# Kernel tuning notes

Measured on AMD Instinct MI355X. Metric: run time of the kernel, lower is better.

Reference implementation:

```python
import jax, jax.numpy as jnp
import numpy as np

SHAPES = ((100, 100), (50, 50), (25, 25))  # (H, W) per level
B, D, NH, HD, NL, NP, DFF = 4, 256, 8, 32, 3, 4, 1024
L = sum(h * w for h, w in SHAPES)  # 13125
EPS = 1e-5


def _layer_norm(x, g, b):
    m = jnp.mean(x, axis=-1, keepdims=True)
    v = jnp.var(x, axis=-1, keepdims=True)
    return (x - m) * jax.lax.rsqrt(v + EPS) * g + b


def _grid_sample_bilinear(img, grid):
    """img: [N,C,H,W]; grid: [N,Lq,P,2] in [-1,1]; align_corners=False, zero pad.
    Returns [N,C,Lq,P]."""
    N, C, H, W = img.shape
    x = ((grid[..., 0] + 1.0) * W - 1.0) * 0.5
    y = ((grid[..., 1] + 1.0) * H - 1.0) * 0.5
    x0 = jnp.floor(x); y0 = jnp.floor(y)
    x1 = x0 + 1.0; y1 = y0 + 1.0
    wx1 = x - x0; wx0 = 1.0 - wx1
    wy1 = y - y0; wy0 = 1.0 - wy1
    flat = img.reshape(N, C, H * W)

    def gather(ix, iy):
        valid = ((ix >= 0) & (ix < W) & (iy >= 0) & (iy < H)).astype(img.dtype)
        ii = (jnp.clip(iy, 0, H - 1).astype(jnp.int32) * W
              + jnp.clip(ix, 0, W - 1).astype(jnp.int32))  # [N,Lq,P]
        idx = jnp.broadcast_to(ii.reshape(N, 1, -1), (N, C, ii.shape[1] * ii.shape[2]))
        vals = jnp.take_along_axis(flat, idx, axis=2).reshape(N, C, ii.shape[1], ii.shape[2])
        return vals * valid[:, None]

    out = (gather(x0, y0) * (wx0 * wy0)[:, None]
           + gather(x1, y0) * (wx1 * wy0)[:, None]
           + gather(x0, y1) * (wx0 * wy1)[:, None]
           + gather(x1, y1) * (wx1 * wy1)[:, None])
    return out


def _ms_deform_attn_core(value, loc, attn):
    """value: [B,L,NH,HD]; loc: [B,Lq,NH,NL,NP,2] in [0,1]; attn: [B,Lq,NH,NL,NP]."""
    Bn, Lq = loc.shape[0], loc.shape[1]
    grids = 2.0 * loc - 1.0
    start = 0
    samples = []
    for lid, (H, W) in enumerate(SHAPES):
        v = value[:, start:start + H * W]            # [B,HW,NH,HD]
        start += H * W
        v = v.transpose(0, 2, 3, 1).reshape(Bn * NH, HD, H, W)
        g = grids[:, :, :, lid].transpose(0, 2, 1, 3, 4).reshape(Bn * NH, Lq, NP, 2)
        samples.append(_grid_sample_bilinear(v, g))  # [B*NH,HD,Lq,NP]
    sv = jnp.stack(samples, axis=-2).reshape(Bn * NH, HD, Lq, NL * NP)
    a = attn.transpose(0, 2, 1, 3, 4).reshape(Bn * NH, 1, Lq, NL * NP)
    out = (sv * a).sum(-1)                            # [B*NH,HD,Lq]
    return out.reshape(Bn, NH * HD, Lq).transpose(0, 2, 1)


def setup_inputs() -> dict:
    key = jax.random.key(0)
    ks = jax.random.split(key, 16)
    f32 = jnp.float32
    inp = {
        'src': jax.random.normal(ks[0], (B, L, D), f32),
        'pos': jax.random.normal(ks[1], (B, L, D), f32),
        'reference_points': jax.random.uniform(ks[2], (B, L, NL, 2), f32),
        'Wv': jax.random.normal(ks[3], (D, D), f32) * 0.02,
        'bv': jnp.zeros((D,), f32),
        'Woff': jax.random.normal(ks[4], (D, NH * NL * NP * 2), f32) * 0.02,
        'boff': jax.random.normal(ks[5], (NH * NL * NP * 2,), f32) * 0.5,
        'Wattn': jax.random.normal(ks[6], (D, NH * NL * NP), f32) * 0.02,
        'battn': jnp.zeros((NH * NL * NP,), f32),
        'Wout': jax.random.normal(ks[7], (D, D), f32) * 0.02,
        'bout': jnp.zeros((D,), f32),
        'g1': jnp.ones((D,), f32), 'b1': jnp.zeros((D,), f32),
        'Wff1': jax.random.normal(ks[8], (D, DFF), f32) * 0.02,
        'bff1': jnp.zeros((DFF,), f32),
        'Wff2': jax.random.normal(ks[9], (DFF, D), f32) * 0.02,
        'bff2': jnp.zeros((D,), f32),
        'g2': jnp.ones((D,), f32), 'b2': jnp.zeros((D,), f32),
    }
    return inp


def reference(src, pos, reference_points, Wv, bv, Woff, boff, Wattn, battn,
              Wout, bout, g1, b1, Wff1, bff1, Wff2, bff2, g2, b2):
    # DeformableTransformerEncoderLayer forward (eval mode: dropout = identity)
    q = src + pos
    value = (src @ Wv + bv).reshape(B, L, NH, HD)
    off = (q @ Woff + boff).reshape(B, L, NH, NL, NP, 2)
    attn = jax.nn.softmax((q @ Wattn + battn).reshape(B, L, NH, NL * NP), axis=-1)
    attn = attn.reshape(B, L, NH, NL, NP)
    norm = jnp.array([[w, h] for h, w in SHAPES], dtype=src.dtype)  # [NL,2] = (W,H)
    loc = reference_points[:, :, None, :, None, :] + off / norm[None, None, None, :, None, :]
    attn_out = _ms_deform_attn_core(value, loc, attn) @ Wout + bout
    x = _layer_norm(src + attn_out, g1, b1)
    ff = jax.nn.relu(x @ Wff1 + bff1) @ Wff2 + bff2
    return _layer_norm(x + ff, g2, b2)
```

## Files before the change

### kernel.cpp

```cpp
#include <hip/hip_runtime.h>


#define BLTOK 52500
#define MP    52608
#define LSP   13125

using short8  = __attribute__((ext_vector_type(8))) short;
using ushort8v= __attribute__((ext_vector_type(8))) unsigned short;
using f32x4   = __attribute__((ext_vector_type(4))) float;
using fl2     = __attribute__((ext_vector_type(2))) float;

__device__ __forceinline__ ushort f2b(float f) {
  union { float f; unsigned u; } x; x.f = f;
  unsigned r = (x.u + 0x7fffu + ((x.u >> 16) & 1u)) >> 16;
  return (ushort)r;
}
__device__ __forceinline__ float b2f(ushort h) {
  union { unsigned u; float f; } x; x.u = ((unsigned)h) << 16;
  return x.f;
}

#define GLDS16(gp, lp) __builtin_amdgcn_global_load_lds( \
    (const __attribute__((address_space(1))) void*)(gp), \
    (__attribute__((address_space(3))) void*)(lp), 16, 0, 0)

__global__ __launch_bounds__(256) void prep_weights(
    const float* __restrict__ Wv, const float* __restrict__ Woff,
    const float* __restrict__ Wattn, const float* __restrict__ Wout,
    const float* __restrict__ Wff1, const float* __restrict__ Wff2,
    const float* __restrict__ boff, const float* __restrict__ battn,
    ushort* __restrict__ wv_t, ushort* __restrict__ wcat_t,
    ushort* __restrict__ wout_t, ushort* __restrict__ wff1_t,
    ushort* __restrict__ wff2_t, float* __restrict__ bcat)
{
  int i = blockIdx.x * 256 + threadIdx.x;
  if (i < 65536) {
    int n = i >> 8, k = i & 255;
    wv_t[i] = f2b(Wv[k * 256 + n]);
    return;
  }
  int j = i - 65536;
  if (j < 98304) {
    int n = j >> 8, k = j & 255;
    float v = (n < 192) ? Woff[k * 192 + n]
            : (n < 288) ? Wattn[k * 96 + (n - 192)] : 0.f;
    wcat_t[j] = f2b(v);
    return;
  }
  j -= 98304;
  if (j < 65536) {
    int n = j >> 8, k = j & 255;
    wout_t[j] = f2b(Wout[k * 256 + n]);
    return;
  }
  j -= 65536;
  if (j < 262144) {
    int n = j >> 8, k = j & 255;
    wff1_t[j] = f2b(Wff1[k * 1024 + n]);
    return;
  }
  j -= 262144;
  if (j < 262144) {
    int n = j >> 10, k = j & 1023;
    wff2_t[j] = f2b(Wff2[k * 256 + n]);
    return;
  }
  j -= 262144;
  if (j < 384) bcat[j] = (j < 192) ? boff[j] : (j < 288) ? battn[j - 192] : 0.f;
}

__global__ __launch_bounds__(256) void prep_act(
    const float* __restrict__ src, const float* __restrict__ pos,
    ushort* __restrict__ src_bf, ushort* __restrict__ q_bf)
{
  const size_t e = ((size_t)blockIdx.x * 256 + threadIdx.x) * 4;
  if (e >= (size_t)MP * 256) return;
  ushort4 sb, qb;
  if (e < (size_t)BLTOK * 256) {
    const float4 s = *(const float4*)(src + e);
    const float4 p = *(const float4*)(pos + e);
    sb.x = f2b(s.x); sb.y = f2b(s.y); sb.z = f2b(s.z); sb.w = f2b(s.w);
    qb.x = f2b(s.x + p.x); qb.y = f2b(s.y + p.y);
    qb.z = f2b(s.z + p.z); qb.w = f2b(s.w + p.w);
  } else {
    sb.x = sb.y = sb.z = sb.w = 0;
    qb.x = qb.y = qb.z = qb.w = 0;
  }
  *(ushort4*)(src_bf + e) = sb;
  *(ushort4*)(q_bf + e) = qb;
}

template <int EPI>
__global__ __launch_bounds__(256) void gemm128(
    const ushort* __restrict__ A, const ushort* __restrict__ Bt,
    const float* __restrict__ bias, const float* __restrict__ addf,
    const ushort* __restrict__ addb, ushort* __restrict__ C,
    int Mact, int Nact, int Nstr, int K)
{
  __shared__ __align__(16) ushort sm[16384];
  ushort* As = sm;
  ushort* Bs = sm + 8192;
  float*  epf = (float*)sm;
  const int tid = threadIdx.x;
  const int wave = tid >> 6, lane = tid & 63;
  const int n0 = blockIdx.x * 128, m0 = blockIdx.y * 128;
  const int srow = lane >> 2, skc = (lane & 3) * 8;
  const ushort* Ag = A + (size_t)(m0 + wave * 32 + srow) * K + skc;
  const ushort* Bg = Bt + (size_t)(n0 + wave * 32 + srow) * K + skc;
  const int quad = lane >> 4, l16 = lane & 15;
  const int wm = (wave & 1) * 64, wn = (wave >> 1) * 64;
  f32x4 acc[4][4] = {};

#define STAGE(buf, kk) { \
    ushort* la = As + (buf) * 4096 + wave * 1024; \
    ushort* lb = Bs + (buf) * 4096 + wave * 1024; \
    GLDS16(Ag + (kk), la); \
    GLDS16(Ag + (kk) + 16 * K, la + 512); \
    GLDS16(Bg + (kk), lb); \
    GLDS16(Bg + (kk) + 16 * K, lb + 512); }

  STAGE(0, 0);
  int cur = 0;
  for (int k0 = 0; k0 < K; k0 += 32) {
    __syncthreads();
    if (k0 + 32 < K) STAGE(cur ^ 1, k0 + 32);
    const ushort* Ab = As + cur * 4096;
    const ushort* Bb = Bs + cur * 4096;
    short8 af[4], bf[4];
#pragma unroll
    for (int i = 0; i < 4; i++)
      af[i] = *(const short8*)(&Ab[(wm + i * 16 + l16) * 32 + quad * 8]);
#pragma unroll
    for (int j = 0; j < 4; j++)
      bf[j] = *(const short8*)(&Bb[(wn + j * 16 + l16) * 32 + quad * 8]);
#pragma unroll
    for (int i = 0; i < 4; i++)
#pragma unroll
      for (int j = 0; j < 4; j++)
        acc[i][j] = __builtin_amdgcn_mfma_f32_16x16x32_bf16(af[i], bf[j],
                                                            acc[i][j], 0, 0, 0);
    cur ^= 1;
  }
#undef STAGE

  for (int half = 0; half < 2; half++) {
    __syncthreads();
    if ((wave & 1) == half) {
#pragma unroll
      for (int i = 0; i < 4; i++)
#pragma unroll
        for (int j = 0; j < 4; j++)
#pragma unroll
          for (int r = 0; r < 4; r++)
            epf[(i * 16 + quad * 4 + r) * 128 + wn + j * 16 + l16] = acc[i][j][r];
    }
    __syncthreads();
    const int gm0 = m0 + half * 64;
#pragma unroll
    for (int g = 0; g < 4; g++) {
      const int lrow = g * 16 + (tid >> 4);
      const int col0 = (tid & 15) * 8;
      const int grow = gm0 + lrow;
      const int gcol = n0 + col0;
      if (grow < Mact && gcol < Nact) {
        float v[8];
#pragma unroll
        for (int c = 0; c < 8; c++) v[c] = epf[lrow * 128 + col0 + c] + bias[gcol + c];
        const size_t idx = (size_t)grow * Nstr + gcol;
        if (EPI == 1) {
          const float4 a0 = *(const float4*)(addf + idx);
          const float4 a1 = *(const float4*)(addf + idx + 4);
          v[0] += a0.x; v[1] += a0.y; v[2] += a0.z; v[3] += a0.w;
          v[4] += a1.x; v[5] += a1.y; v[6] += a1.z; v[7] += a1.w;
        }
        if (EPI == 2) {
#pragma unroll
          for (int c = 0; c < 8; c++) v[c] = fmaxf(v[c], 0.f);
        }
        if (EPI == 3) {
          const ushort8v ab = *(const ushort8v*)(addb + idx);
#pragma unroll
          for (int c = 0; c < 8; c++) v[c] += b2f(ab[c]);
        }
        ushort8v o;
#pragma unroll
        for (int c = 0; c < 8; c++) o[c] = f2b(v[c]);
        *(ushort8v*)(C + idx) = o;
      }
    }
  }
}

__global__ __launch_bounds__(256) void softmax12(ushort* __restrict__ offattn)
{
  const int t = blockIdx.x * 256 + threadIdx.x;
  if (t >= BLTOK * 8) return;
  const int r = t >> 3, h = t & 7;
  ushort* p = offattn + (size_t)r * 320 + 192 + h * 12;
  float v[12], mx = -1e30f;
#pragma unroll
  for (int i = 0; i < 12; i++) { v[i] = b2f(p[i]); mx = fmaxf(mx, v[i]); }
  float s = 0.f;
#pragma unroll
  for (int i = 0; i < 12; i++) { v[i] = expf(v[i] - mx); s += v[i]; }
  const float inv = 1.f / s;
#pragma unroll
  for (int i = 0; i < 12; i++) p[i] = f2b(v[i] * inv);
}

__global__ __launch_bounds__(256) void deform_sample(
    const ushort* __restrict__ value, const ushort* __restrict__ oa_all,
    const float* __restrict__ refp, ushort* __restrict__ outb)
{
  const int tid = threadIdx.x;
  const int tok = blockIdx.x * 8 + (tid >> 5);
  if (tok >= BLTOK) return;
  const int b = tok / LSP;
  const int l = tid & 31;
  const int h = l >> 2;
  const ushort* oa = oa_all + (uint)tok * 320u;
  const float* rp = refp + (uint)tok * 6u;
  const uint base = (uint)b * (LSP * 256u) + (uint)(l * 8);
  const int Wl[3] = {100, 50, 25};
  const int Stl[3] = {0, 10000, 12500};
  fl2 acc2[4] = {};
#pragma unroll
  for (int lid = 0; lid < 3; lid++) {
    const int W = Wl[lid], st = Stl[lid];
    const float Wf = (float)W;
    const float rx = rp[lid * 2], ry = rp[lid * 2 + 1];
#pragma unroll
    for (int p = 0; p < 4; p++) {
      const uint oxy = *(const uint*)(oa + h * 24 + lid * 8 + p * 2);
      union { uint u; float f; } ux, uy;
      ux.u = oxy << 16;
      uy.u = oxy & 0xffff0000u;
      const float aw = b2f(oa[192 + h * 12 + lid * 4 + p]);
      const float x = (rx + ux.f / Wf) * Wf - 0.5f;
      const float y = (ry + uy.f / Wf) * Wf - 0.5f;
      const float x0f = floorf(x), y0f = floorf(y);
      const float wx1 = x - x0f, wy1 = y - y0f;
      const float wx0 = 1.f - wx1, wy0 = 1.f - wy1;
      const int ix0 = (int)x0f, iy0 = (int)y0f;
      const bool x0v = (ix0 >= 0) & (ix0 < W);
      const bool x1v = (ix0 + 1 >= 0) & (ix0 + 1 < W);
      const bool y0v = (iy0 >= 0) & (iy0 < W);
      const bool y1v = (iy0 + 1 >= 0) & (iy0 + 1 < W);
      const float ay0 = aw * wy0, ay1 = aw * wy1;
      const float w00 = (x0v & y0v) ? ay0 * wx0 : 0.f;
      const float w10 = (x1v & y0v) ? ay0 * wx1 : 0.f;
      const float w01 = (x0v & y1v) ? ay1 * wx0 : 0.f;
      const float w11 = (x1v & y1v) ? ay1 * wx1 : 0.f;
      const int ix0c = min(max(ix0, 0), W - 1);
      const int ix1c = min(max(ix0 + 1, 0), W - 1);
      const int iy0c = min(max(iy0, 0), W - 1);
      const int iy1c = min(max(iy0 + 1, 0), W - 1);
      const uint r00 = (uint)(st + iy0c * W + ix0c) * 256u;
      const uint r10 = (uint)(st + iy0c * W + ix1c) * 256u;
      const uint r01 = (uint)(st + iy1c * W + ix0c) * 256u;
      const uint r11 = (uint)(st + iy1c * W + ix1c) * 256u;
      const uint4 q00 = *(const uint4*)(value + base + r00);
      const uint4 q10 = *(const uint4*)(value + base + r10);
      const uint4 q01 = *(const uint4*)(value + base + r01);
      const uint4 q11 = *(const uint4*)(value + base + r11);
      const fl2 w00v = {w00, w00}, w10v = {w10, w10};
      const fl2 w01v = {w01, w01}, w11v = {w11, w11};
      const uint* u00 = (const uint*)&q00;
      const uint* u10 = (const uint*)&q10;
      const uint* u01 = (const uint*)&q01;
      const uint* u11 = (const uint*)&q11;
#pragma unroll
      for (int pp = 0; pp < 4; pp++) {
        union { uint u; float f; } a, bb2, cc, dd, a2, b2u, c2, d2;
        a.u  = u00[pp] << 16;  a2.u  = u00[pp] & 0xffff0000u;
        bb2.u= u10[pp] << 16;  b2u.u = u10[pp] & 0xffff0000u;
        cc.u = u01[pp] << 16;  c2.u  = u01[pp] & 0xffff0000u;
        dd.u = u11[pp] << 16;  d2.u  = u11[pp] & 0xffff0000u;
        fl2 v00 = {a.f, a2.f}, v10 = {bb2.f, b2u.f};
        fl2 v01 = {cc.f, c2.f}, v11 = {dd.f, d2.f};
        acc2[pp] += w00v * v00 + w10v * v10 + w01v * v01 + w11v * v11;
      }
    }
  }
  ushort4 o0, o1;
  o0.x = f2b(acc2[0].x); o0.y = f2b(acc2[0].y);
  o0.z = f2b(acc2[1].x); o0.w = f2b(acc2[1].y);
  o1.x = f2b(acc2[2].x); o1.y = f2b(acc2[2].y);
  o1.z = f2b(acc2[3].x); o1.w = f2b(acc2[3].y);
  ushort* op = outb + (uint)tok * 256u + (uint)(l * 8);
  *(ushort4*)op = o0;
  *(ushort4*)(op + 4) = o1;
}

template <int OUTF>
__global__ __launch_bounds__(256) void ln256(
    const ushort* __restrict__ in, const float* __restrict__ gg,
    const float* __restrict__ bb, ushort* __restrict__ outb,
    float* __restrict__ outf, int rows)
{
  const int wave = threadIdx.x >> 6, lane = threadIdx.x & 63;
  const int r = blockIdx.x * 4 + wave;
  if (r >= rows) return;
  const ushort* rowp = in + (size_t)r * 256;
  const ushort4 u = *(const ushort4*)(rowp + lane * 4);
  float v[4] = {b2f(u.x), b2f(u.y), b2f(u.z), b2f(u.w)};
  float s = v[0] + v[1] + v[2] + v[3];
  float s2 = v[0] * v[0] + v[1] * v[1] + v[2] * v[2] + v[3] * v[3];
#pragma unroll
  for (int o = 32; o > 0; o >>= 1) {
    s += __shfl_xor(s, o);
    s2 += __shfl_xor(s2, o);
  }
  const float mean = s * (1.f / 256.f);
  const float var = s2 * (1.f / 256.f) - mean * mean;
  const float rstd = rsqrtf(var + 1e-5f);
#pragma unroll
  for (int j = 0; j < 4; j++) {
    const int col = lane * 4 + j;
    const float o = (v[j] - mean) * rstd * gg[col] + bb[col];
    if (OUTF) outf[(size_t)r * 256 + col] = o;
    else outb[(size_t)r * 256 + col] = f2b(o);
  }
}

extern "C" void kernel_launch(void* const* d_in, const int* in_sizes, int n_in,
                              void* d_out, int out_size, void* d_ws, size_t ws_size,
                              hipStream_t stream)
{
  const float* src   = (const float*)d_in[0];
  const float* pos   = (const float*)d_in[1];
  const float* refp  = (const float*)d_in[2];
  const float* Wv    = (const float*)d_in[3];
  const float* bv    = (const float*)d_in[4];
  const float* Woff  = (const float*)d_in[5];
  const float* boff  = (const float*)d_in[6];
  const float* Wattn = (const float*)d_in[7];
  const float* battn = (const float*)d_in[8];
  const float* Wout  = (const float*)d_in[9];
  const float* bout  = (const float*)d_in[10];
  const float* g1    = (const float*)d_in[11];
  const float* b1    = (const float*)d_in[12];
  const float* Wff1  = (const float*)d_in[13];
  const float* bff1  = (const float*)d_in[14];
  const float* Wff2  = (const float*)d_in[15];
  const float* bff2  = (const float*)d_in[16];
  const float* g2    = (const float*)d_in[17];
  const float* b2    = (const float*)d_in[18];
  float* out = (float*)d_out;
  char* ws = (char*)d_ws;

  ushort* wcat_t = (ushort*)(ws + 0);
  ushort* wff1_t = (ushort*)(ws + 196608);
  ushort* wff2_t = (ushort*)(ws + 720896);
  float*  bcat   = (float*)(ws + 1245184);
  ushort* A1 = (ushort*)(ws + 1246720);
  ushort* A2 = (ushort*)(ws + 28182016);
  ushort* A3 = (ushort*)(ws + 55117312);
  ushort* A4 = (ushort*)(ws + 81997312);
  ushort* A5 = (ushort*)(ws + 115597312);
  ushort* wout_t = (ushort*)(ws + 223076352);
  ushort* wv_t   = (ushort*)(ws + 223207424);

  prep_weights<<<2946, 256, 0, stream>>>(Wv, Woff, Wattn, Wout, Wff1, Wff2,
                                         boff, battn,
                                         wv_t, wcat_t, wout_t, wff1_t, wff2_t, bcat);
  prep_act<<<MP / 4, 256, 0, stream>>>(src, pos, A1, A2);
  gemm128<0><<<dim3(2, MP / 128), 256, 0, stream>>>(A1, wv_t, bv, nullptr, nullptr,
                                                    A3, BLTOK, 256, 256, 256);
  gemm128<0><<<dim3(3, MP / 128), 256, 0, stream>>>(A2, wcat_t, bcat, nullptr, nullptr,
                                                    A4, BLTOK, 320, 320, 256);
  softmax12<<<(BLTOK * 8 + 255) / 256, 256, 0, stream>>>(A4);
  deform_sample<<<(BLTOK + 7) / 8, 256, 0, stream>>>(A3, A4, refp, A5);
  gemm128<3><<<dim3(2, MP / 128), 256, 0, stream>>>(A5, wout_t, bout, nullptr, A1,
                                                    A4, BLTOK, 256, 256, 256);
  ln256<0><<<BLTOK / 4, 256, 0, stream>>>(A4, g1, b1, A2, nullptr, BLTOK);
  gemm128<2><<<dim3(8, MP / 128), 256, 0, stream>>>(A2, wff1_t, bff1, nullptr, nullptr,
                                                    A5, MP, 1024, 1024, 256);
  gemm128<3><<<dim3(2, MP / 128), 256, 0, stream>>>(A5, wff2_t, bff2, nullptr, A2,
                                                    A3, BLTOK, 256, 256, 1024);
  ln256<1><<<BLTOK / 4, 256, 0, stream>>>(A3, g2, b2, nullptr, out, BLTOK);
}
```

Measured before the change: 484.3 us.

## Fuse softmax into deform sampling and remap threads to one head each

Removes the separate softmax12 kernel and computes the per-head softmax over the 12 attention logits inside deform_sample. Each thread now handles one head's 32 channels of one token instead of 8 channels, so offsets, weights and bilinear indices are computed once per head rather than four times. The location math is simplified to ref*W - 0.5 + offset. Blocks are reordered so each group stays within one batch, which should help L2 locality. The trade-off is higher register pressure (16 accumulators plus 16-byte loads per corner) and a different memory access pattern for the value gathers.

```diff
diff --git a/kernel.cpp b/kernel.cpp
--- a/kernel.cpp
+++ b/kernel.cpp
@@ -18,6 +18,12 @@
 __device__ __forceinline__ float b2f(ushort h) {
   union { unsigned u; float f; } x; x.u = ((unsigned)h) << 16;
   return x.f;
+}
+__device__ __forceinline__ float lo16f(uint u) {
+  union { unsigned u; float f; } x; x.u = u << 16; return x.f;
+}
+__device__ __forceinline__ float hi16f(uint u) {
+  union { unsigned u; float f; } x; x.u = u & 0xffff0000u; return x.f;
 }
 
 #define GLDS16(gp, lp) __builtin_amdgcn_global_load_lds( \
@@ -191,53 +197,66 @@
   }
 }
 
-__global__ __launch_bounds__(256) void softmax12(ushort* __restrict__ offattn)
-{
-  const int t = blockIdx.x * 256 + threadIdx.x;
-  if (t >= BLTOK * 8) return;
-  const int r = t >> 3, h = t & 7;
-  ushort* p = offattn + (size_t)r * 320 + 192 + h * 12;
-  float v[12], mx = -1e30f;
-#pragma unroll
-  for (int i = 0; i < 12; i++) { v[i] = b2f(p[i]); mx = fmaxf(mx, v[i]); }
-  float s = 0.f;
-#pragma unroll
-  for (int i = 0; i < 12; i++) { v[i] = expf(v[i] - mx); s += v[i]; }
-  const float inv = 1.f / s;
-#pragma unroll
-  for (int i = 0; i < 12; i++) p[i] = f2b(v[i] * inv);
-}
-
 __global__ __launch_bounds__(256) void deform_sample(
     const ushort* __restrict__ value, const ushort* __restrict__ oa_all,
     const float* __restrict__ refp, ushort* __restrict__ outb)
 {
   const int tid = threadIdx.x;
-  const int tok = blockIdx.x * 8 + (tid >> 5);
-  if (tok >= BLTOK) return;
-  const int b = tok / LSP;
-  const int l = tid & 31;
-  const int h = l >> 2;
-  const ushort* oa = oa_all + (uint)tok * 320u;
-  const float* rp = refp + (uint)tok * 6u;
-  const uint base = (uint)b * (LSP * 256u) + (uint)(l * 8);
+  const int g = blockIdx.x & 7, j = blockIdx.x >> 3;
+  const int batch = g >> 1;
+  const int tin = ((g & 1) * 206 + j) * 32 + (tid >> 3);
+  if (tin >= LSP) return;
+  const int tok = batch * LSP + tin;
+  const int h = tid & 7;
+  const ushort* oa = oa_all + (size_t)tok * 320;
+  uint offv[12];
+  {
+    const uint4 o0 = *(const uint4*)(oa + h * 24);
+    const uint4 o1 = *(const uint4*)(oa + h * 24 + 8);
+    const uint4 o2 = *(const uint4*)(oa + h * 24 + 16);
+    offv[0] = o0.x; offv[1] = o0.y; offv[2] = o0.z; offv[3] = o0.w;
+    offv[4] = o1.x; offv[5] = o1.y; offv[6] = o1.z; offv[7] = o1.w;
+    offv[8] = o2.x; offv[9] = o2.y; offv[10] = o2.z; offv[11] = o2.w;
+  }
+  float wsm[12];
+  {
+    const ushort* lg = oa + 192 + h * 12;
+    const uint2 l0 = *(const uint2*)(lg);
+    const uint2 l1 = *(const uint2*)(lg + 4);
+    const uint2 l2 = *(const uint2*)(lg + 8);
+    wsm[0] = lo16f(l0.x); wsm[1] = hi16f(l0.x);
+    wsm[2] = lo16f(l0.y); wsm[3] = hi16f(l0.y);
+    wsm[4] = lo16f(l1.x); wsm[5] = hi16f(l1.x);
+    wsm[6] = lo16f(l1.y); wsm[7] = hi16f(l1.y);
+    wsm[8] = lo16f(l2.x); wsm[9] = hi16f(l2.x);
+    wsm[10] = lo16f(l2.y); wsm[11] = hi16f(l2.y);
+    float mx = wsm[0];
+#pragma unroll
+    for (int i = 1; i < 12; i++) mx = fmaxf(mx, wsm[i]);
+    float s = 0.f;
+#pragma unroll
+    for (int i = 0; i < 12; i++) { wsm[i] = __expf(wsm[i] - mx); s += wsm[i]; }
+    const float inv = 1.f / s;
+#pragma unroll
+    for (int i = 0; i < 12; i++) wsm[i] *= inv;
+  }
+  const float* rp = refp + (size_t)tok * 6;
+  const uint vbase = (uint)batch * (LSP * 256u) + (uint)(h * 32);
   const int Wl[3] = {100, 50, 25};
   const int Stl[3] = {0, 10000, 12500};
-  fl2 acc2[4] = {};
+  fl2 acc2[16] = {};
 #pragma unroll
   for (int lid = 0; lid < 3; lid++) {
     const int W = Wl[lid], st = Stl[lid];
     const float Wf = (float)W;
-    const float rx = rp[lid * 2], ry = rp[lid * 2 + 1];
+    const float bx = rp[lid * 2] * Wf - 0.5f;
+    const float by = rp[lid * 2 + 1] * Wf - 0.5f;
 #pragma unroll
     for (int p = 0; p < 4; p++) {
-      const uint oxy = *(const uint*)(oa + h * 24 + lid * 8 + p * 2);
-      union { uint u; float f; } ux, uy;
-      ux.u = oxy << 16;
-      uy.u = oxy & 0xffff0000u;
-      const float aw = b2f(oa[192 + h * 12 + lid * 4 + p]);
-      const float x = (rx + ux.f / Wf) * Wf - 0.5f;
-      const float y = (ry + uy.f / Wf) * Wf - 0.5f;
+      const uint oxy = offv[lid * 4 + p];
+      const float x = bx + lo16f(oxy);
+      const float y = by + hi16f(oxy);
+      const float aw = wsm[lid * 4 + p];
       const float x0f = floorf(x), y0f = floorf(y);
       const float wx1 = x - x0f, wy1 = y - y0f;
       const float wx0 = 1.f - wx1, wy0 = 1.f - wy1;
@@ -255,41 +274,63 @@
       const int ix1c = min(max(ix0 + 1, 0), W - 1);
       const int iy0c = min(max(iy0, 0), W - 1);
       const int iy1c = min(max(iy0 + 1, 0), W - 1);
-      const uint r00 = (uint)(st + iy0c * W + ix0c) * 256u;
-      const uint r10 = (uint)(st + iy0c * W + ix1c) * 256u;
-      const uint r01 = (uint)(st + iy1c * W + ix0c) * 256u;
-      const uint r11 = (uint)(st + iy1c * W + ix1c) * 256u;
-      const uint4 q00 = *(const uint4*)(value + base + r00);
-      const uint4 q10 = *(const uint4*)(value + base + r10);
-      const uint4 q01 = *(const uint4*)(value + base + r01);
-      const uint4 q11 = *(const uint4*)(value + base + r11);
+      const uint r00 = vbase + (uint)(st + iy0c * W + ix0c) * 256u;
+      const uint r10 = vbase + (uint)(st + iy0c * W + ix1c) * 256u;
+      const uint r01 = vbase + (uint)(st + iy1c * W + ix0c) * 256u;
+      const uint r11 = vbase + (uint)(st + iy1c * W + ix1c) * 256u;
+      uint4 q00[2], q10[2], q01[2], q11[2];
+#pragma unroll
+      for (int c = 0; c < 2; c++) {
+        q00[c] = *(const uint4*)(value + r00 + c * 8);
+        q10[c] = *(const uint4*)(value + r10 + c * 8);
+        q01[c] = *(const uint4*)(value + r01 + c * 8);
+        q11[c] = *(const uint4*)(value + r11 + c * 8);
+      }
       const fl2 w00v = {w00, w00}, w10v = {w10, w10};
       const fl2 w01v = {w01, w01}, w11v = {w11, w11};
-      const uint* u00 = (const uint*)&q00;
-      const uint* u10 = (const uint*)&q10;
-      const uint* u01 = (const uint*)&q01;
-      const uint* u11 = (const uint*)&q11;
-#pragma unroll
-      for (int pp = 0; pp < 4; pp++) {
-        union { uint u; float f; } a, bb2, cc, dd, a2, b2u, c2, d2;
-        a.u  = u00[pp] << 16;  a2.u  = u00[pp] & 0xffff0000u;
-        bb2.u= u10[pp] << 16;  b2u.u = u10[pp] & 0xffff0000u;
-        cc.u = u01[pp] << 16;  c2.u  = u01[pp] & 0xffff0000u;
-        dd.u = u11[pp] << 16;  d2.u  = u11[pp] & 0xffff0000u;
-        fl2 v00 = {a.f, a2.f}, v10 = {bb2.f, b2u.f};
-        fl2 v01 = {cc.f, c2.f}, v11 = {dd.f, d2.f};
-        acc2[pp] += w00v * v00 + w10v * v10 + w01v * v01 + w11v * v11;
+      const uint* u00 = (const uint*)q00;
+      const uint* u10 = (const uint*)q10;
+      const uint* u01 = (const uint*)q01;
+      const uint* u11 = (const uint*)q11;
+#pragma unroll
+      for (int d = 0; d < 8; d++) {
+        fl2 v00 = {lo16f(u00[d]), hi16f(u00[d])};
+        fl2 v10 = {lo16f(u10[d]), hi16f(u10[d])};
+        fl2 v01 = {lo16f(u01[d]), hi16f(u01[d])};
+        fl2 v11 = {lo16f(u11[d]), hi16f(u11[d])};
+        acc2[d] += w00v * v00 + w10v * v10 + w01v * v01 + w11v * v11;
+      }
+      uint4 q00b[2], q10b[2], q01b[2], q11b[2];
+#pragma unroll
+      for (int c = 0; c < 2; c++) {
+        q00b[c] = *(const uint4*)(value + r00 + 16 + c * 8);
+        q10b[c] = *(const uint4*)(value + r10 + 16 + c * 8);
+        q01b[c] = *(const uint4*)(value + r01 + 16 + c * 8);
+        q11b[c] = *(const uint4*)(value + r11 + 16 + c * 8);
+      }
+      const uint* v00p = (const uint*)q00b;
+      const uint* v10p = (const uint*)q10b;
+      const uint* v01p = (const uint*)q01b;
+      const uint* v11p = (const uint*)q11b;
+#pragma unroll
+      for (int d = 0; d < 8; d++) {
+        fl2 v00 = {lo16f(v00p[d]), hi16f(v00p[d])};
+        fl2 v10 = {lo16f(v10p[d]), hi16f(v10p[d])};
+        fl2 v01 = {lo16f(v01p[d]), hi16f(v01p[d])};
+        fl2 v11 = {lo16f(v11p[d]), hi16f(v11p[d])};
+        acc2[8 + d] += w00v * v00 + w10v * v10 + w01v * v01 + w11v * v11;
       }
     }
   }
-  ushort4 o0, o1;
-  o0.x = f2b(acc2[0].x); o0.y = f2b(acc2[0].y);
-  o0.z = f2b(acc2[1].x); o0.w = f2b(acc2[1].y);
-  o1.x = f2b(acc2[2].x); o1.y = f2b(acc2[2].y);
-  o1.z = f2b(acc2[3].x); o1.w = f2b(acc2[3].y);
-  ushort* op = outb + (uint)tok * 256u + (uint)(l * 8);
-  *(ushort4*)op = o0;
-  *(ushort4*)(op + 4) = o1;
+  uint ov[16];
+#pragma unroll
+  for (int d = 0; d < 16; d++)
+    ov[d] = (uint)f2b(acc2[d].x) | ((uint)f2b(acc2[d].y) << 16);
+  ushort* op = outb + (size_t)tok * 256 + h * 32;
+  *(uint4*)(op) = *(uint4*)(ov);
+  *(uint4*)(op + 8) = *(uint4*)(ov + 4);
+  *(uint4*)(op + 16) = *(uint4*)(ov + 8);
+  *(uint4*)(op + 24) = *(uint4*)(ov + 12);
 }
 
 template <int OUTF>
@@ -369,8 +410,7 @@
                                                     A3, BLTOK, 256, 256, 256);
   gemm128<0><<<dim3(3, MP / 128), 256, 0, stream>>>(A2, wcat_t, bcat, nullptr, nullptr,
                                                     A4, BLTOK, 320, 320, 256);
-  softmax12<<<(BLTOK * 8 + 255) / 256, 256, 0, stream>>>(A4);
-  deform_sample<<<(BLTOK + 7) / 8, 256, 0, stream>>>(A3, A4, refp, A5);
+  deform_sample<<<8 * 206, 256, 0, stream>>>(A3, A4, refp, A5);
   gemm128<3><<<dim3(2, MP / 128), 256, 0, stream>>>(A5, wout_t, bout, nullptr, A1,
                                                     A4, BLTOK, 256, 256, 256);
   ln256<0><<<BLTOK / 4, 256, 0, stream>>>(A4, g1, b1, A2, nullptr, BLTOK);
```

After: 607.3 us. 25.4% more time.

## Switch GEMMs to 64x256 tiles, trim M padding, simplify deform sampling math

Applied to the files above, without the earlier changes.

Replaces the 128x128 GEMM tile with a 64x256 tile in which each of the four waves owns a 64x64 slice and all waves share one A tile. M padding shrinks to a multiple of 64, and prep_act no longer writes zero padding rows. Padded rows now hold stale workspace data, and the bias-concat GEMM reads weight rows past its real extent; both are masked only by the output bounds checks. The softmax switches to the fast __expf intrinsic, and the deformable sampler precomputes the reference offset per level so it no longer divides and multiplies by W for each point.

```diff
diff --git a/kernel.cpp b/kernel.cpp
--- a/kernel.cpp
+++ b/kernel.cpp
@@ -2,7 +2,7 @@
 
 
 #define BLTOK 52500
-#define MP    52608
+#define MPAD  52544
 #define LSP   13125
 
 using short8  = __attribute__((ext_vector_type(8))) short;
@@ -18,6 +18,12 @@
 __device__ __forceinline__ float b2f(ushort h) {
   union { unsigned u; float f; } x; x.u = ((unsigned)h) << 16;
   return x.f;
+}
+__device__ __forceinline__ float lo16f(uint u) {
+  union { unsigned u; float f; } x; x.u = u << 16; return x.f;
+}
+__device__ __forceinline__ float hi16f(uint u) {
+  union { unsigned u; float f; } x; x.u = u & 0xffff0000u; return x.f;
 }
 
 #define GLDS16(gp, lp) __builtin_amdgcn_global_load_lds( \
@@ -74,62 +80,56 @@
     ushort* __restrict__ src_bf, ushort* __restrict__ q_bf)
 {
   const size_t e = ((size_t)blockIdx.x * 256 + threadIdx.x) * 4;
-  if (e >= (size_t)MP * 256) return;
+  const float4 s = *(const float4*)(src + e);
+  const float4 p = *(const float4*)(pos + e);
   ushort4 sb, qb;
-  if (e < (size_t)BLTOK * 256) {
-    const float4 s = *(const float4*)(src + e);
-    const float4 p = *(const float4*)(pos + e);
-    sb.x = f2b(s.x); sb.y = f2b(s.y); sb.z = f2b(s.z); sb.w = f2b(s.w);
-    qb.x = f2b(s.x + p.x); qb.y = f2b(s.y + p.y);
-    qb.z = f2b(s.z + p.z); qb.w = f2b(s.w + p.w);
-  } else {
-    sb.x = sb.y = sb.z = sb.w = 0;
-    qb.x = qb.y = qb.z = qb.w = 0;
-  }
+  sb.x = f2b(s.x); sb.y = f2b(s.y); sb.z = f2b(s.z); sb.w = f2b(s.w);
+  qb.x = f2b(s.x + p.x); qb.y = f2b(s.y + p.y);
+  qb.z = f2b(s.z + p.z); qb.w = f2b(s.w + p.w);
   *(ushort4*)(src_bf + e) = sb;
   *(ushort4*)(q_bf + e) = qb;
 }
 
 template <int EPI>
-__global__ __launch_bounds__(256) void gemm128(
+__global__ __launch_bounds__(256) void gemm64n(
     const ushort* __restrict__ A, const ushort* __restrict__ Bt,
-    const float* __restrict__ bias, const float* __restrict__ addf,
-    const ushort* __restrict__ addb, ushort* __restrict__ C,
-    int Mact, int Nact, int Nstr, int K)
-{
-  __shared__ __align__(16) ushort sm[16384];
+    const float* __restrict__ bias, const ushort* __restrict__ addb,
+    ushort* __restrict__ C, int Mact, int Nact, int Nstr, int K)
+{
+  __shared__ __align__(16) ushort sm[20480];
   ushort* As = sm;
-  ushort* Bs = sm + 8192;
+  ushort* Bs = sm + 4096;
   float*  epf = (float*)sm;
   const int tid = threadIdx.x;
   const int wave = tid >> 6, lane = tid & 63;
-  const int n0 = blockIdx.x * 128, m0 = blockIdx.y * 128;
+  const int n0 = blockIdx.x * 256, m0 = blockIdx.y * 64;
   const int srow = lane >> 2, skc = (lane & 3) * 8;
-  const ushort* Ag = A + (size_t)(m0 + wave * 32 + srow) * K + skc;
-  const ushort* Bg = Bt + (size_t)(n0 + wave * 32 + srow) * K + skc;
+  const ushort* Ag = A + (size_t)(m0 + wave * 16 + srow) * K + skc;
+  const ushort* Bg = Bt + (size_t)(n0 + wave * 64 + srow) * K + skc;
   const int quad = lane >> 4, l16 = lane & 15;
-  const int wm = (wave & 1) * 64, wn = (wave >> 1) * 64;
+  const int wn = wave * 64;
   f32x4 acc[4][4] = {};
 
 #define STAGE(buf, kk) { \
-    ushort* la = As + (buf) * 4096 + wave * 1024; \
-    ushort* lb = Bs + (buf) * 4096 + wave * 1024; \
+    ushort* la = As + (buf) * 2048 + wave * 512; \
+    ushort* lb = Bs + (buf) * 8192 + wave * 2048; \
     GLDS16(Ag + (kk), la); \
-    GLDS16(Ag + (kk) + 16 * K, la + 512); \
     GLDS16(Bg + (kk), lb); \
-    GLDS16(Bg + (kk) + 16 * K, lb + 512); }
+    GLDS16(Bg + (kk) + 16 * K, lb + 512); \
+    GLDS16(Bg + (kk) + 32 * K, lb + 1024); \
+    GLDS16(Bg + (kk) + 48 * K, lb + 1536); }
 
   STAGE(0, 0);
   int cur = 0;
   for (int k0 = 0; k0 < K; k0 += 32) {
     __syncthreads();
     if (k0 + 32 < K) STAGE(cur ^ 1, k0 + 32);
-    const ushort* Ab = As + cur * 4096;
-    const ushort* Bb = Bs + cur * 4096;
+    const ushort* Ab = As + cur * 2048;
+    const ushort* Bb = Bs + cur * 8192;
     short8 af[4], bf[4];
 #pragma unroll
     for (int i = 0; i < 4; i++)
-      af[i] = *(const short8*)(&Ab[(wm + i * 16 + l16) * 32 + quad * 8]);
+      af[i] = *(const short8*)(&Ab[(i * 16 + l16) * 32 + quad * 8]);
 #pragma unroll
     for (int j = 0; j < 4; j++)
       bf[j] = *(const short8*)(&Bb[(wn + j * 16 + l16) * 32 + quad * 8]);
@@ -143,36 +143,29 @@
   }
 #undef STAGE
 
-  for (int half = 0; half < 2; half++) {
+  for (int q = 0; q < 2; q++) {
     __syncthreads();
-    if ((wave & 1) == half) {
-#pragma unroll
-      for (int i = 0; i < 4; i++)
-#pragma unroll
-        for (int j = 0; j < 4; j++)
-#pragma unroll
-          for (int r = 0; r < 4; r++)
-            epf[(i * 16 + quad * 4 + r) * 128 + wn + j * 16 + l16] = acc[i][j][r];
+#pragma unroll
+    for (int ii = 0; ii < 2; ii++) {
+      const int i = q * 2 + ii;
+#pragma unroll
+      for (int j = 0; j < 4; j++)
+#pragma unroll
+        for (int r = 0; r < 4; r++)
+          epf[(ii * 16 + quad * 4 + r) * 256 + wn + j * 16 + l16] = acc[i][j][r];
     }
     __syncthreads();
-    const int gm0 = m0 + half * 64;
 #pragma unroll
     for (int g = 0; g < 4; g++) {
-      const int lrow = g * 16 + (tid >> 4);
-      const int col0 = (tid & 15) * 8;
-      const int grow = gm0 + lrow;
+      const int lrow = g * 8 + (tid >> 5);
+      const int col0 = (tid & 31) * 8;
+      const int grow = m0 + q * 32 + lrow;
       const int gcol = n0 + col0;
       if (grow < Mact && gcol < Nact) {
         float v[8];
 #pragma unroll
-        for (int c = 0; c < 8; c++) v[c] = epf[lrow * 128 + col0 + c] + bias[gcol + c];
+        for (int c = 0; c < 8; c++) v[c] = epf[lrow * 256 + col0 + c] + bias[gcol + c];
         const size_t idx = (size_t)grow * Nstr + gcol;
-        if (EPI == 1) {
-          const float4 a0 = *(const float4*)(addf + idx);
-          const float4 a1 = *(const float4*)(addf + idx + 4);
-          v[0] += a0.x; v[1] += a0.y; v[2] += a0.z; v[3] += a0.w;
-          v[4] += a1.x; v[5] += a1.y; v[6] += a1.z; v[7] += a1.w;
-        }
         if (EPI == 2) {
 #pragma unroll
           for (int c = 0; c < 8; c++) v[c] = fmaxf(v[c], 0.f);
@@ -202,7 +195,7 @@
   for (int i = 0; i < 12; i++) { v[i] = b2f(p[i]); mx = fmaxf(mx, v[i]); }
   float s = 0.f;
 #pragma unroll
-  for (int i = 0; i < 12; i++) { v[i] = expf(v[i] - mx); s += v[i]; }
+  for (int i = 0; i < 12; i++) { v[i] = __expf(v[i] - mx); s += v[i]; }
   const float inv = 1.f / s;
 #pragma unroll
   for (int i = 0; i < 12; i++) p[i] = f2b(v[i] * inv);
@@ -228,16 +221,14 @@
   for (int lid = 0; lid < 3; lid++) {
     const int W = Wl[lid], st = Stl[lid];
     const float Wf = (float)W;
-    const float rx = rp[lid * 2], ry = rp[lid * 2 + 1];
+    const float bx = rp[lid * 2] * Wf - 0.5f;
+    const float by = rp[lid * 2 + 1] * Wf - 0.5f;
 #pragma unroll
     for (int p = 0; p < 4; p++) {
       const uint oxy = *(const uint*)(oa + h * 24 + lid * 8 + p * 2);
-      union { uint u; float f; } ux, uy;
-      ux.u = oxy << 16;
-      uy.u = oxy & 0xffff0000u;
       const float aw = b2f(oa[192 + h * 12 + lid * 4 + p]);
-      const float x = (rx + ux.f / Wf) * Wf - 0.5f;
-      const float y = (ry + uy.f / Wf) * Wf - 0.5f;
+      const float x = bx + lo16f(oxy);
+      const float y = by + hi16f(oxy);
       const float x0f = floorf(x), y0f = floorf(y);
       const float wx1 = x - x0f, wy1 = y - y0f;
       const float wx0 = 1.f - wx1, wy0 = 1.f - wy1;
@@ -271,13 +262,10 @@
       const uint* u11 = (const uint*)&q11;
 #pragma unroll
       for (int pp = 0; pp < 4; pp++) {
-        union { uint u; float f; } a, bb2, cc, dd, a2, b2u, c2, d2;
-        a.u  = u00[pp] << 16;  a2.u  = u00[pp] & 0xffff0000u;
-        bb2.u= u10[pp] << 16;  b2u.u = u10[pp] & 0xffff0000u;
-        cc.u = u01[pp] << 16;  c2.u  = u01[pp] & 0xffff0000u;
-        dd.u = u11[pp] << 16;  d2.u  = u11[pp] & 0xffff0000u;
-        fl2 v00 = {a.f, a2.f}, v10 = {bb2.f, b2u.f};
-        fl2 v01 = {cc.f, c2.f}, v11 = {dd.f, d2.f};
+        fl2 v00 = {lo16f(u00[pp]), hi16f(u00[pp])};
+        fl2 v10 = {lo16f(u10[pp]), hi16f(u10[pp])};
+        fl2 v01 = {lo16f(u01[pp]), hi16f(u01[pp])};
+        fl2 v11 = {lo16f(u11[pp]), hi16f(u11[pp])};
         acc2[pp] += w00v * v00 + w10v * v10 + w01v * v01 + w11v * v11;
       }
     }
@@ -354,29 +342,29 @@
   ushort* wff2_t = (ushort*)(ws + 720896);
   float*  bcat   = (float*)(ws + 1245184);
   ushort* A1 = (ushort*)(ws + 1246720);
-  ushort* A2 = (ushort*)(ws + 28182016);
-  ushort* A3 = (ushort*)(ws + 55117312);
-  ushort* A4 = (ushort*)(ws + 81997312);
-  ushort* A5 = (ushort*)(ws + 115597312);
-  ushort* wout_t = (ushort*)(ws + 223076352);
-  ushort* wv_t   = (ushort*)(ws + 223207424);
+  ushort* A2 = (ushort*)(ws + 28126720);
+  ushort* A3 = (ushort*)(ws + 55006720);
+  ushort* A4 = (ushort*)(ws + 81886720);
+  ushort* A5 = (ushort*)(ws + 115486720);
+  ushort* wv_t   = (ushort*)(ws + 155486720);
+  ushort* wout_t = (ushort*)(ws + 155617792);
 
   prep_weights<<<2946, 256, 0, stream>>>(Wv, Woff, Wattn, Wout, Wff1, Wff2,
                                          boff, battn,
                                          wv_t, wcat_t, wout_t, wff1_t, wff2_t, bcat);
-  prep_act<<<MP / 4, 256, 0, stream>>>(src, pos, A1, A2);
-  gemm128<0><<<dim3(2, MP / 128), 256, 0, stream>>>(A1, wv_t, bv, nullptr, nullptr,
-                                                    A3, BLTOK, 256, 256, 256);
-  gemm128<0><<<dim3(3, MP / 128), 256, 0, stream>>>(A2, wcat_t, bcat, nullptr, nullptr,
-                                                    A4, BLTOK, 320, 320, 256);
+  prep_act<<<BLTOK / 4, 256, 0, stream>>>(src, pos, A1, A2);
+  gemm64n<0><<<dim3(1, MPAD / 64), 256, 0, stream>>>(A1, wv_t, bv, nullptr,
+                                                     A3, BLTOK, 256, 256, 256);
+  gemm64n<0><<<dim3(2, MPAD / 64), 256, 0, stream>>>(A2, wcat_t, bcat, nullptr,
+                                                     A4, BLTOK, 320, 320, 256);
   softmax12<<<(BLTOK * 8 + 255) / 256, 256, 0, stream>>>(A4);
   deform_sample<<<(BLTOK + 7) / 8, 256, 0, stream>>>(A3, A4, refp, A5);
-  gemm128<3><<<dim3(2, MP / 128), 256, 0, stream>>>(A5, wout_t, bout, nullptr, A1,
-                                                    A4, BLTOK, 256, 256, 256);
+  gemm64n<3><<<dim3(1, MPAD / 64), 256, 0, stream>>>(A5, wout_t, bout, A1,
+                                                     A4, BLTOK, 256, 256, 256);
   ln256<0><<<BLTOK / 4, 256, 0, stream>>>(A4, g1, b1, A2, nullptr, BLTOK);
-  gemm128<2><<<dim3(8, MP / 128), 256, 0, stream>>>(A2, wff1_t, bff1, nullptr, nullptr,
-                                                    A5, MP, 1024, 1024, 256);
-  gemm128<3><<<dim3(2, MP / 128), 256, 0, stream>>>(A5, wff2_t, bff2, nullptr, A2,
-                                                    A3, BLTOK, 256, 256, 1024);
+  gemm64n<2><<<dim3(4, MPAD / 64), 256, 0, stream>>>(A2, wff1_t, bff1, nullptr,
+                                                     A5, BLTOK, 1024, 1024, 256);
+  gemm64n<3><<<dim3(1, MPAD / 64), 256, 0, stream>>>(A5, wff2_t, bff2, A2,
+                                                     A3, BLTOK, 256, 256, 1024);
   ln256<1><<<BLTOK / 4, 256, 0, stream>>>(A3, g2, b2, nullptr, out, BLTOK);
 }
```

New measurement: 488.4 us. Within noise of the previous version (+0.8%).
